# Performance work log

Hardware: AMD Instinct MI355X
Metric: run time of the kernel (lower is better)

Reference implementation:

```python
import jax, jax.numpy as jnp
import numpy as np

R = 16            # filter radius (init kwarg r)
EPS = 0.01        # regularizer (init kwarg eps)
B, H, W, C, K = 2, 1024, 1024, 3, 4


def _make_kernel():
    # Gaussian kernel with theta_alpha = r/4, center tap zeroed (as in source)
    x, y = np.mgrid[-R:R + 1, -R:R + 1]
    theta = R / 4.0
    k = np.exp(-0.5 * (x ** 2 + y ** 2) / theta ** 2).astype(np.float32)
    k[R, R] = 0.0
    return jnp.asarray(k)


def setup_inputs() -> dict:
    key = jax.random.key(0)
    k1, k2 = jax.random.split(key)
    I = jax.random.uniform(k1, (B, H, W, C), dtype=jnp.float32)
    p = jax.random.uniform(k2, (B, H, W, K), dtype=jnp.float32)
    return {"I": I, "p": p}


def _gaussian_filter(src, kfft):
    # FFT-based 'same' convolution with the (2R+1)^2 Gaussian kernel over (h, w).
    # src: [b, h, w, *trailing]; filtering applied independently per trailing channel.
    shp = src.shape
    b, h, w = shp[0], shp[1], shp[2]
    s = src.reshape(b, h, w, -1)
    s = jnp.pad(s, ((0, 0), (R, R), (R, R), (0, 0)))          # [b, h+2R, w+2R, c]
    sf = jnp.fft.rfft2(s, axes=(1, 2))
    d = jnp.fft.irfft2(sf * kfft[None, :, :, None], s=(h + 2 * R, w + 2 * R), axes=(1, 2))
    d = d[:, 2 * R:, 2 * R:, :]                               # crop back to [b, h, w, c]
    return d.reshape(shp)


def _guided_filter(I, p):
    b, h, w, c = I.shape
    k = _make_kernel()
    ext_k = jnp.pad(k, ((0, h - 1), (0, w - 1)))              # [h+2R, w+2R]
    kfft = jnp.fft.rfft2(ext_k)
    gf = lambda x: _gaussian_filter(x, kfft)

    N = gf(jnp.ones((1, h, w, 1), I.dtype))                   # normalization map
    mean_I = gf(I) / N                                        # [b,h,w,c]
    mean_p = gf(p) / N                                        # [b,h,w,k]
    # cov(I, p): [b,h,w,c,k]
    cov_Ip = gf(I[..., :, None] * p[..., None, :]) / N[..., None] \
        - mean_I[..., :, None] * mean_p[..., None, :]
    # var(I): [b,h,w,c,c]
    var_I = gf(I[..., :, None] * I[..., None, :]) / N[..., None] \
        - mean_I[..., :, None] * mean_I[..., None, :]
    A = var_I + EPS * jnp.eye(c, dtype=I.dtype)
    a = jnp.linalg.solve(A, cov_Ip)                           # == inv(A) @ cov_Ip, [b,h,w,c,k]
    b_ = mean_p[..., None] - jnp.einsum('bhwck,bhwc->bhwk', a, mean_I)[..., None]  # [b,h,w,k,1]
    mean_a = gf(a) / N[..., None]
    mean_b = gf(b_) / N[..., None]
    q = jnp.einsum('bhwck,bhwc->bhwk', mean_a, I)[..., None] + mean_b
    return q.reshape(p.shape)


def reference(I, p):
    return _guided_filter(I, p)
```

## Files before the change

kernel.cpp:

```cpp
#include <hip/hip_runtime.h>


#define HH 1024
#define WW 1024
#define HWSZ (HH * WW)
#define RR 16
#define NT 33
#define EPSF 0.01f

#define VBY 32
#define VROWS (VBY + 2 * RR)
#define VCOLS 256

typedef unsigned short u16;
typedef unsigned int u32;
typedef float v2f __attribute__((ext_vector_type(2)));

__device__ constexpr float WG[NT] = {
  0.000335463f, 0.000883827f, 0.002187492f, 0.005086072f, 0.011108997f,
  0.022794173f, 0.043936928f, 0.079559512f, 0.135335283f, 0.216265076f,
  0.324652467f, 0.457833362f, 0.606530660f, 0.754839602f, 0.882496903f,
  0.969233234f, 1.0f,         0.969233234f, 0.882496903f, 0.754839602f,
  0.606530660f, 0.457833362f, 0.324652467f, 0.216265076f, 0.135335283f,
  0.079559512f, 0.043936928f, 0.022794173f, 0.011108997f, 0.005086072f,
  0.002187492f, 0.000883827f, 0.000335463f
};

__device__ constexpr float wg_sum() {
  float s = 0.0f;
  for (int i = 0; i < NT; ++i) s += WG[i];
  return s;
}

__device__ __forceinline__ u16 f2bf(float f) {
  u32 u = __float_as_uint(f);
  u += 0x7fffu + ((u >> 16) & 1u);
  return (u16)(u >> 16);
}
__device__ __forceinline__ float bf2f(u16 v) { return __uint_as_float(((u32)v) << 16); }

__device__ __forceinline__ float win_w(int u, int n) {
  constexpr float S = wg_sum();
  if (u >= RR && u < n - RR) return S;
  float w = 0.0f;
#pragma unroll
  for (int i = 0; i < NT; ++i) {
    const int uu = u - RR + i;
    if (uu >= 0 && uu < n) w += WG[i];
  }
  return w;
}

__global__ __launch_bounds__(256) void k_prod_hblur(const float* __restrict__ I,
                                                    const float* __restrict__ P,
                                                    u16* __restrict__ HB) {
  __shared__ float sI[3][288];
  __shared__ float sp[4][288];
  const int tid = threadIdx.x;
  const int y = blockIdx.y;
  const int x0 = blockIdx.x * 256;
  {
    const int base = (y * WW + (x0 - RR)) * 3;
    for (int idx = tid; idx < 288 * 3; idx += 256) {
      const int xi = idx / 3;
      const int c = idx - xi * 3;
      const int xx = x0 - RR + xi;
      sI[c][xi] = (xx >= 0 && xx < WW) ? I[base + idx] : 0.0f;
    }
  }
  {
    const int base = (y * WW + (x0 - RR)) * 4;
    for (int idx = tid; idx < 288 * 4; idx += 256) {
      const int xi = idx >> 2;
      const int c = idx & 3;
      const int xx = x0 - RR + xi;
      sp[c][xi] = (xx >= 0 && xx < WW) ? P[base + idx] : 0.0f;
    }
  }
  __syncthreads();

  float acc[25];
#pragma unroll
  for (int j = 0; j < 25; ++j) acc[j] = 0.0f;

#pragma unroll
  for (int dx = 0; dx < NT; ++dx) {
    const float w = WG[dx];
    const float i0 = sI[0][tid + dx], i1 = sI[1][tid + dx], i2 = sI[2][tid + dx];
    const float p0 = sp[0][tid + dx], p1 = sp[1][tid + dx];
    const float p2 = sp[2][tid + dx], p3 = sp[3][tid + dx];
    const float wi0 = w * i0, wi1 = w * i1, wi2 = w * i2;
    const float wp0 = w * p0, wp1 = w * p1, wp2 = w * p2, wp3 = w * p3;
    acc[0] += wi0; acc[1] += wi1; acc[2] += wi2;
    acc[3] += wp0; acc[4] += wp1; acc[5] += wp2; acc[6] += wp3;
    acc[7]  += i0 * wp0; acc[8]  += i0 * wp1; acc[9]  += i0 * wp2; acc[10] += i0 * wp3;
    acc[11] += i1 * wp0; acc[12] += i1 * wp1; acc[13] += i1 * wp2; acc[14] += i1 * wp3;
    acc[15] += i2 * wp0; acc[16] += i2 * wp1; acc[17] += i2 * wp2; acc[18] += i2 * wp3;
    acc[19] += wi0 * i0; acc[20] += wi0 * i1; acc[21] += wi0 * i2;
    acc[22] += wi1 * i1; acc[23] += wi1 * i2; acc[24] += wi2 * i2;
  }
  const int o = y * WW + x0 + tid;
#pragma unroll
  for (int ch = 0; ch < 25; ++ch) HB[ch * HWSZ + o] = f2bf(acc[ch]);
}

__global__ __launch_bounds__(256) void k_vblur25(const u16* __restrict__ HB,
                                                 u16* __restrict__ M) {
  __shared__ u16 s[VROWS][VCOLS];
  const int tid = threadIdx.x;
  const int ch = blockIdx.z;
  const int xb = blockIdx.x * VCOLS;
  const int y0 = blockIdx.y * VBY;
  const int x = xb + tid;

  {
    const u16* src = HB + (size_t)ch * HWSZ + xb;
    uint4 tmp[8];
#pragma unroll
    for (int it = 0; it < 8; ++it) {
      const int id = it * 256 + tid;
      const int row = id >> 5;
      const int cir = id & 31;
      const int gy = y0 - RR + row;
      uint4 v = make_uint4(0u, 0u, 0u, 0u);
      if (gy >= 0 && gy < HH)
        v = *reinterpret_cast<const uint4*>(src + (size_t)gy * WW + cir * 8);
      tmp[it] = v;
    }
#pragma unroll
    for (int it = 0; it < 8; ++it) {
      const int id = it * 256 + tid;
      const int row = id >> 5;
      const int cir = id & 31;
      *reinterpret_cast<uint4*>(&s[row][cir * 8]) = tmp[it];
    }
  }
  __syncthreads();

  u16* dst = M + (size_t)ch * HWSZ;

  for (int c = 0; c < 4; ++c) {
    v2f a[4];
#pragma unroll
    for (int q = 0; q < 4; ++q) a[q] = (v2f){0.0f, 0.0f};
#pragma unroll
    for (int r = 0; r < 40; ++r) {
      const float v = bf2f(s[8 * c + r][tid]);
#pragma unroll
      for (int q = 0; q < 4; ++q) {
        const int dy0 = r - 2 * q;
        const int dy1 = r - 2 * q - 1;
        const float wa = (dy0 >= 0 && dy0 < NT) ? WG[dy0] : 0.0f;
        const float wb = (dy1 >= 0 && dy1 < NT) ? WG[dy1] : 0.0f;
        if (wa != 0.0f || wb != 0.0f) {
          const v2f w = {wa, wb};
          a[q] += w * v;
        }
      }
    }
#pragma unroll
    for (int q = 0; q < 4; ++q) {
      const int yy = y0 + 8 * c + 2 * q;
      dst[yy * WW + x] = f2bf(a[q].x);
      dst[(yy + 1) * WW + x] = f2bf(a[q].y);
    }
  }
}

__global__ __launch_bounds__(256) void k_solve(const u16* __restrict__ M,
                                               const float* __restrict__ I,
                                               const float* __restrict__ P,
                                               float* __restrict__ AB,
                                               float* __restrict__ S0) {
  const int i = blockIdx.x * 256 + threadIdx.x;
  const int y = i >> 10;
  const int x = i & 1023;
  const float invN = __builtin_amdgcn_rcpf(win_w(x, WW) * win_w(y, HH) - 1.0f);

  const float I0 = I[i * 3], I1 = I[i * 3 + 1], I2 = I[i * 3 + 2];
  float p[4];
#pragma unroll
  for (int k = 0; k < 4; ++k) p[k] = P[i * 4 + k];

  const float mI0 = (bf2f(M[i]) - I0) * invN;
  const float mI1 = (bf2f(M[HWSZ + i]) - I1) * invN;
  const float mI2 = (bf2f(M[2 * HWSZ + i]) - I2) * invN;
  float mp[4];
#pragma unroll
  for (int k = 0; k < 4; ++k) mp[k] = (bf2f(M[(3 + k) * HWSZ + i]) - p[k]) * invN;
  float cov[12];
#pragma unroll
  for (int k = 0; k < 4; ++k) {
    cov[k]     = (bf2f(M[(7 + k) * HWSZ + i])  - I0 * p[k]) * invN - mI0 * mp[k];
    cov[4 + k] = (bf2f(M[(11 + k) * HWSZ + i]) - I1 * p[k]) * invN - mI1 * mp[k];
    cov[8 + k] = (bf2f(M[(15 + k) * HWSZ + i]) - I2 * p[k]) * invN - mI2 * mp[k];
  }
  const float A00 = (bf2f(M[19 * HWSZ + i]) - I0 * I0) * invN - mI0 * mI0 + EPSF;
  const float A01 = (bf2f(M[20 * HWSZ + i]) - I0 * I1) * invN - mI0 * mI1;
  const float A02 = (bf2f(M[21 * HWSZ + i]) - I0 * I2) * invN - mI0 * mI2;
  const float A11 = (bf2f(M[22 * HWSZ + i]) - I1 * I1) * invN - mI1 * mI1 + EPSF;
  const float A12 = (bf2f(M[23 * HWSZ + i]) - I1 * I2) * invN - mI1 * mI2;
  const float A22 = (bf2f(M[24 * HWSZ + i]) - I2 * I2) * invN - mI2 * mI2 + EPSF;
  const float c00 = A11 * A22 - A12 * A12;
  const float c01 = A02 * A12 - A01 * A22;
  const float c02 = A01 * A12 - A02 * A11;
  const float det = A00 * c00 + A01 * c01 + A02 * c02;
  const float idet = 1.0f / det;
  const float i00 = c00 * idet, i01 = c01 * idet, i02 = c02 * idet;
  const float i11 = (A00 * A22 - A02 * A02) * idet;
  const float i12 = (A01 * A02 - A00 * A12) * idet;
  const float i22 = (A00 * A11 - A01 * A01) * idet;
  float4 s0;
  float* s0p = &s0.x;
#pragma unroll
  for (int k = 0; k < 4; ++k) {
    const float a0 = i00 * cov[k] + i01 * cov[4 + k] + i02 * cov[8 + k];
    const float a1 = i01 * cov[k] + i11 * cov[4 + k] + i12 * cov[8 + k];
    const float a2 = i02 * cov[k] + i12 * cov[4 + k] + i22 * cov[8 + k];
    const float b = mp[k] - (a0 * mI0 + a1 * mI1 + a2 * mI2);
    AB[k * HWSZ + i] = a0;
    AB[(4 + k) * HWSZ + i] = a1;
    AB[(8 + k) * HWSZ + i] = a2;
    AB[(12 + k) * HWSZ + i] = b;
    s0p[k] = a0 * I0 + a1 * I1 + a2 * I2 + b;
  }
  *reinterpret_cast<float4*>(S0 + (size_t)i * 4) = s0;
}

__global__ __launch_bounds__(256) void k_hblur16(const float* __restrict__ AB,
                                                 u16* __restrict__ HB) {
  __shared__ float s[1056];
  const int tid = threadIdx.x;
  const int y = blockIdx.x;
  const int ch = blockIdx.y;
  const float* src = AB + (size_t)ch * HWSZ + y * WW;
  if (tid < 16) { s[tid] = 0.0f; s[1040 + tid] = 0.0f; }
  *reinterpret_cast<float4*>(&s[16 + 4 * tid]) =
      *reinterpret_cast<const float4*>(&src[4 * tid]);
  __syncthreads();

  float vals[36];
  {
    const float4* s4 = reinterpret_cast<const float4*>(s) + tid;
#pragma unroll
    for (int r = 0; r < 9; ++r) {
      const float4 q = s4[r];
      vals[4 * r] = q.x; vals[4 * r + 1] = q.y;
      vals[4 * r + 2] = q.z; vals[4 * r + 3] = q.w;
    }
  }
  float acc[4] = {0.0f, 0.0f, 0.0f, 0.0f};
#pragma unroll
  for (int r = 0; r < 36; ++r) {
#pragma unroll
    for (int k = 0; k < 4; ++k) {
      const int dy = r - k;
      if (dy >= 0 && dy < NT) acc[k] += WG[dy] * vals[r];
    }
  }
  const u32 lo = (u32)f2bf(acc[0]) | ((u32)f2bf(acc[1]) << 16);
  const u32 hi = (u32)f2bf(acc[2]) | ((u32)f2bf(acc[3]) << 16);
  *reinterpret_cast<uint2*>(&HB[(size_t)ch * HWSZ + y * WW + 4 * tid]) =
      make_uint2(lo, hi);
}

__global__ __launch_bounds__(256) void k_vblur16(const u16* __restrict__ HB,
                                                 u16* __restrict__ MB) {
  __shared__ u16 s[VROWS][VCOLS];
  const int tid = threadIdx.x;
  const int ch = blockIdx.z;
  const int xb = blockIdx.x * VCOLS;
  const int y0 = blockIdx.y * VBY;
  const int x = xb + tid;

  {
    const u16* src = HB + (size_t)ch * HWSZ + xb;
    uint4 tmp[8];
#pragma unroll
    for (int it = 0; it < 8; ++it) {
      const int id = it * 256 + tid;
      const int row = id >> 5;
      const int cir = id & 31;
      const int gy = y0 - RR + row;
      uint4 v = make_uint4(0u, 0u, 0u, 0u);
      if (gy >= 0 && gy < HH)
        v = *reinterpret_cast<const uint4*>(src + (size_t)gy * WW + cir * 8);
      tmp[it] = v;
    }
#pragma unroll
    for (int it = 0; it < 8; ++it) {
      const int id = it * 256 + tid;
      const int row = id >> 5;
      const int cir = id & 31;
      *reinterpret_cast<uint4*>(&s[row][cir * 8]) = tmp[it];
    }
  }
  __syncthreads();

  u16* dst = MB + (size_t)ch * HWSZ;

  for (int c = 0; c < 4; ++c) {
    v2f a[4];
#pragma unroll
    for (int q = 0; q < 4; ++q) a[q] = (v2f){0.0f, 0.0f};
#pragma unroll
    for (int r = 0; r < 40; ++r) {
      const float v = bf2f(s[8 * c + r][tid]);
#pragma unroll
      for (int q = 0; q < 4; ++q) {
        const int dy0 = r - 2 * q;
        const int dy1 = r - 2 * q - 1;
        const float wa = (dy0 >= 0 && dy0 < NT) ? WG[dy0] : 0.0f;
        const float wb = (dy1 >= 0 && dy1 < NT) ? WG[dy1] : 0.0f;
        if (wa != 0.0f || wb != 0.0f) {
          const v2f w = {wa, wb};
          a[q] += w * v;
        }
      }
    }
#pragma unroll
    for (int q = 0; q < 4; ++q) {
      const int yy = y0 + 8 * c + 2 * q;
      dst[yy * WW + x] = f2bf(a[q].x);
      dst[(yy + 1) * WW + x] = f2bf(a[q].y);
    }
  }
}

__global__ __launch_bounds__(256) void k_combine(const u16* __restrict__ MB,
                                                 const float* __restrict__ S0,
                                                 const float* __restrict__ I,
                                                 float* __restrict__ out) {
  const int i = blockIdx.x * 256 + threadIdx.x;
  const int y = i >> 10;
  const int x = i & 1023;
  const float invN = __builtin_amdgcn_rcpf(win_w(x, WW) * win_w(y, HH) - 1.0f);
  float m[16];
#pragma unroll
  for (int ch = 0; ch < 16; ++ch) m[ch] = bf2f(MB[(size_t)ch * HWSZ + i]);
  const float i0 = I[i * 3], i1 = I[i * 3 + 1], i2 = I[i * 3 + 2];
  const float4 s0 = *reinterpret_cast<const float4*>(S0 + (size_t)i * 4);
  float4 q;
  q.x = (m[0] * i0 + m[4] * i1 + m[8]  * i2 + m[12] - s0.x) * invN;
  q.y = (m[1] * i0 + m[5] * i1 + m[9]  * i2 + m[13] - s0.y) * invN;
  q.z = (m[2] * i0 + m[6] * i1 + m[10] * i2 + m[14] - s0.z) * invN;
  q.w = (m[3] * i0 + m[7] * i1 + m[11] * i2 + m[15] - s0.w) * invN;
  *reinterpret_cast<float4*>(out + (size_t)i * 4) = q;
}

extern "C" void kernel_launch(void* const* d_in, const int* in_sizes, int n_in,
                              void* d_out, int out_size, void* d_ws, size_t ws_size,
                              hipStream_t stream) {
  const float* I = (const float*)d_in[0];
  const float* P = (const float*)d_in[1];
  float* out = (float*)d_out;
  float* buf0 = (float*)d_ws;
  float* buf1 = buf0 + 25 * (size_t)HWSZ;

  u16* hb1 = (u16*)buf0;
  u16* Mb  = (u16*)buf1;
  float* AB = buf0;
  float* S0 = buf0 + 16 * (size_t)HWSZ;
  u16* hb2 = (u16*)buf1;
  u16* MBp = (u16*)buf1 + 16 * (size_t)HWSZ;

  for (int b = 0; b < 2; ++b) {
    const float* Ib = I + (size_t)b * HWSZ * 3;
    const float* Pb = P + (size_t)b * HWSZ * 4;
    float* outb = out + (size_t)b * HWSZ * 4;

    k_prod_hblur<<<dim3(WW / 256, HH), dim3(256), 0, stream>>>(Ib, Pb, hb1);
    k_vblur25<<<dim3(WW / VCOLS, HH / VBY, 25), dim3(256), 0, stream>>>(hb1, Mb);
    k_solve<<<dim3(HWSZ / 256), dim3(256), 0, stream>>>(Mb, Ib, Pb, AB, S0);
    k_hblur16<<<dim3(HH, 16), dim3(256), 0, stream>>>(AB, hb2);
    k_vblur16<<<dim3(WW / VCOLS, HH / VBY, 16), dim3(256), 0, stream>>>(hb2, MBp);
    k_combine<<<dim3(HWSZ / 256), dim3(256), 0, stream>>>(MBp, S0, Ib, outb);
  }
}
```

Measured before the change: 299.3 us.

## Split product computation from horizontal blur and store intermediates in bf16

The fused product-plus-horizontal-blur kernel is replaced by a separate pointwise kernel that writes all 25 product planes in bf16, followed by a generic bf16 horizontal blur shared with the second pass. The solve kernel now writes the a/b coefficients as bf16 instead of fp32, which halves that traffic, and the two vertical-blur kernels are merged into one. The aim is to drop the heavy per-tap product arithmetic and strided input loads of the fused kernel. In exchange it adds an extra full write and read of 25 bf16 planes plus one more launch per batch, and it rounds the products and coefficients to bf16 before blurring, which costs accuracy.

```diff
diff --git a/kernel.cpp b/kernel.cpp
--- a/kernel.cpp
+++ b/kernel.cpp
@@ -51,61 +51,84 @@
   return w;
 }
 
-__global__ __launch_bounds__(256) void k_prod_hblur(const float* __restrict__ I,
-                                                    const float* __restrict__ P,
-                                                    u16* __restrict__ HB) {
-  __shared__ float sI[3][288];
-  __shared__ float sp[4][288];
+__global__ __launch_bounds__(256) void k_products(const float* __restrict__ I,
+                                                  const float* __restrict__ P,
+                                                  u16* __restrict__ PR) {
+  const int t = blockIdx.x * 256 + threadIdx.x;
+  const float2* i2 = reinterpret_cast<const float2*>(I);
+  const float2 a = i2[3 * t], b = i2[3 * t + 1], c = i2[3 * t + 2];
+  const float4* p4 = reinterpret_cast<const float4*>(P);
+  const float4 q0 = p4[2 * t], q1 = p4[2 * t + 1];
+
+  const float iA[3] = {a.x, a.y, b.x};
+  const float iB[3] = {b.y, c.x, c.y};
+  const float pA[4] = {q0.x, q0.y, q0.z, q0.w};
+  const float pB[4] = {q1.x, q1.y, q1.z, q1.w};
+
+  u32* dst = reinterpret_cast<u32*>(PR) + t;
+  const int half = HWSZ / 2;
+#define ST(ch, va, vb) dst[(ch) * half] = (u32)f2bf(va) | ((u32)f2bf(vb) << 16)
+  ST(0, iA[0], iB[0]); ST(1, iA[1], iB[1]); ST(2, iA[2], iB[2]);
+  ST(3, pA[0], pB[0]); ST(4, pA[1], pB[1]); ST(5, pA[2], pB[2]); ST(6, pA[3], pB[3]);
+#pragma unroll
+  for (int cc = 0; cc < 3; ++cc)
+#pragma unroll
+    for (int k = 0; k < 4; ++k)
+      ST(7 + cc * 4 + k, iA[cc] * pA[k], iB[cc] * pB[k]);
+  ST(19, iA[0] * iA[0], iB[0] * iB[0]);
+  ST(20, iA[0] * iA[1], iB[0] * iB[1]);
+  ST(21, iA[0] * iA[2], iB[0] * iB[2]);
+  ST(22, iA[1] * iA[1], iB[1] * iB[1]);
+  ST(23, iA[1] * iA[2], iB[1] * iB[2]);
+  ST(24, iA[2] * iA[2], iB[2] * iB[2]);
+#undef ST
+}
+
+template <int NPL>
+__global__ __launch_bounds__(256) void k_hblur_bf(const u16* __restrict__ SRC,
+                                                  u16* __restrict__ DST) {
+  __shared__ float s[1056];
   const int tid = threadIdx.x;
-  const int y = blockIdx.y;
-  const int x0 = blockIdx.x * 256;
+  const int y = blockIdx.x;
+  const int ch = blockIdx.y;
+  const u16* src = SRC + (size_t)ch * HWSZ + y * WW;
+  if (tid < 16) { s[tid] = 0.0f; s[1040 + tid] = 0.0f; }
   {
-    const int base = (y * WW + (x0 - RR)) * 3;
-    for (int idx = tid; idx < 288 * 3; idx += 256) {
-      const int xi = idx / 3;
-      const int c = idx - xi * 3;
-      const int xx = x0 - RR + xi;
-      sI[c][xi] = (xx >= 0 && xx < WW) ? I[base + idx] : 0.0f;
-    }
-  }
+    const uint2 v = *reinterpret_cast<const uint2*>(src + 4 * tid);
+    s[16 + 4 * tid]     = bf2f((u16)v.x);
+    s[16 + 4 * tid + 1] = bf2f((u16)(v.x >> 16));
+    s[16 + 4 * tid + 2] = bf2f((u16)v.y);
+    s[16 + 4 * tid + 3] = bf2f((u16)(v.y >> 16));
+  }
+  __syncthreads();
+
+  float vals[36];
   {
-    const int base = (y * WW + (x0 - RR)) * 4;
-    for (int idx = tid; idx < 288 * 4; idx += 256) {
-      const int xi = idx >> 2;
-      const int c = idx & 3;
-      const int xx = x0 - RR + xi;
-      sp[c][xi] = (xx >= 0 && xx < WW) ? P[base + idx] : 0.0f;
-    }
-  }
-  __syncthreads();
-
-  float acc[25];
-#pragma unroll
-  for (int j = 0; j < 25; ++j) acc[j] = 0.0f;
-
-#pragma unroll
-  for (int dx = 0; dx < NT; ++dx) {
-    const float w = WG[dx];
-    const float i0 = sI[0][tid + dx], i1 = sI[1][tid + dx], i2 = sI[2][tid + dx];
-    const float p0 = sp[0][tid + dx], p1 = sp[1][tid + dx];
-    const float p2 = sp[2][tid + dx], p3 = sp[3][tid + dx];
-    const float wi0 = w * i0, wi1 = w * i1, wi2 = w * i2;
-    const float wp0 = w * p0, wp1 = w * p1, wp2 = w * p2, wp3 = w * p3;
-    acc[0] += wi0; acc[1] += wi1; acc[2] += wi2;
-    acc[3] += wp0; acc[4] += wp1; acc[5] += wp2; acc[6] += wp3;
-    acc[7]  += i0 * wp0; acc[8]  += i0 * wp1; acc[9]  += i0 * wp2; acc[10] += i0 * wp3;
-    acc[11] += i1 * wp0; acc[12] += i1 * wp1; acc[13] += i1 * wp2; acc[14] += i1 * wp3;
-    acc[15] += i2 * wp0; acc[16] += i2 * wp1; acc[17] += i2 * wp2; acc[18] += i2 * wp3;
-    acc[19] += wi0 * i0; acc[20] += wi0 * i1; acc[21] += wi0 * i2;
-    acc[22] += wi1 * i1; acc[23] += wi1 * i2; acc[24] += wi2 * i2;
-  }
-  const int o = y * WW + x0 + tid;
-#pragma unroll
-  for (int ch = 0; ch < 25; ++ch) HB[ch * HWSZ + o] = f2bf(acc[ch]);
-}
-
-__global__ __launch_bounds__(256) void k_vblur25(const u16* __restrict__ HB,
-                                                 u16* __restrict__ M) {
+    const float4* s4 = reinterpret_cast<const float4*>(s) + tid;
+#pragma unroll
+    for (int r = 0; r < 9; ++r) {
+      const float4 q = s4[r];
+      vals[4 * r] = q.x; vals[4 * r + 1] = q.y;
+      vals[4 * r + 2] = q.z; vals[4 * r + 3] = q.w;
+    }
+  }
+  float acc[4] = {0.0f, 0.0f, 0.0f, 0.0f};
+#pragma unroll
+  for (int r = 0; r < 36; ++r) {
+#pragma unroll
+    for (int k = 0; k < 4; ++k) {
+      const int dy = r - k;
+      if (dy >= 0 && dy < NT) acc[k] += WG[dy] * vals[r];
+    }
+  }
+  const u32 lo = (u32)f2bf(acc[0]) | ((u32)f2bf(acc[1]) << 16);
+  const u32 hi = (u32)f2bf(acc[2]) | ((u32)f2bf(acc[3]) << 16);
+  *reinterpret_cast<uint2*>(&DST[(size_t)ch * HWSZ + y * WW + 4 * tid]) =
+      make_uint2(lo, hi);
+}
+
+__global__ __launch_bounds__(256) void k_vblur(const u16* __restrict__ HB,
+                                               u16* __restrict__ M) {
   __shared__ u16 s[VROWS][VCOLS];
   const int tid = threadIdx.x;
   const int ch = blockIdx.z;
@@ -170,7 +193,7 @@
 __global__ __launch_bounds__(256) void k_solve(const u16* __restrict__ M,
                                                const float* __restrict__ I,
                                                const float* __restrict__ P,
-                                               float* __restrict__ AB,
+                                               u16* __restrict__ AB,
                                                float* __restrict__ S0) {
   const int i = blockIdx.x * 256 + threadIdx.x;
   const int y = i >> 10;
@@ -218,113 +241,13 @@
     const float a1 = i01 * cov[k] + i11 * cov[4 + k] + i12 * cov[8 + k];
     const float a2 = i02 * cov[k] + i12 * cov[4 + k] + i22 * cov[8 + k];
     const float b = mp[k] - (a0 * mI0 + a1 * mI1 + a2 * mI2);
-    AB[k * HWSZ + i] = a0;
-    AB[(4 + k) * HWSZ + i] = a1;
-    AB[(8 + k) * HWSZ + i] = a2;
-    AB[(12 + k) * HWSZ + i] = b;
+    AB[k * HWSZ + i] = f2bf(a0);
+    AB[(4 + k) * HWSZ + i] = f2bf(a1);
+    AB[(8 + k) * HWSZ + i] = f2bf(a2);
+    AB[(12 + k) * HWSZ + i] = f2bf(b);
     s0p[k] = a0 * I0 + a1 * I1 + a2 * I2 + b;
   }
   *reinterpret_cast<float4*>(S0 + (size_t)i * 4) = s0;
-}
-
-__global__ __launch_bounds__(256) void k_hblur16(const float* __restrict__ AB,
-                                                 u16* __restrict__ HB) {
-  __shared__ float s[1056];
-  const int tid = threadIdx.x;
-  const int y = blockIdx.x;
-  const int ch = blockIdx.y;
-  const float* src = AB + (size_t)ch * HWSZ + y * WW;
-  if (tid < 16) { s[tid] = 0.0f; s[1040 + tid] = 0.0f; }
-  *reinterpret_cast<float4*>(&s[16 + 4 * tid]) =
-      *reinterpret_cast<const float4*>(&src[4 * tid]);
-  __syncthreads();
-
-  float vals[36];
-  {
-    const float4* s4 = reinterpret_cast<const float4*>(s) + tid;
-#pragma unroll
-    for (int r = 0; r < 9; ++r) {
-      const float4 q = s4[r];
-      vals[4 * r] = q.x; vals[4 * r + 1] = q.y;
-      vals[4 * r + 2] = q.z; vals[4 * r + 3] = q.w;
-    }
-  }
-  float acc[4] = {0.0f, 0.0f, 0.0f, 0.0f};
-#pragma unroll
-  for (int r = 0; r < 36; ++r) {
-#pragma unroll
-    for (int k = 0; k < 4; ++k) {
-      const int dy = r - k;
-      if (dy >= 0 && dy < NT) acc[k] += WG[dy] * vals[r];
-    }
-  }
-  const u32 lo = (u32)f2bf(acc[0]) | ((u32)f2bf(acc[1]) << 16);
-  const u32 hi = (u32)f2bf(acc[2]) | ((u32)f2bf(acc[3]) << 16);
-  *reinterpret_cast<uint2*>(&HB[(size_t)ch * HWSZ + y * WW + 4 * tid]) =
-      make_uint2(lo, hi);
-}
-
-__global__ __launch_bounds__(256) void k_vblur16(const u16* __restrict__ HB,
-                                                 u16* __restrict__ MB) {
-  __shared__ u16 s[VROWS][VCOLS];
-  const int tid = threadIdx.x;
-  const int ch = blockIdx.z;
-  const int xb = blockIdx.x * VCOLS;
-  const int y0 = blockIdx.y * VBY;
-  const int x = xb + tid;
-
-  {
-    const u16* src = HB + (size_t)ch * HWSZ + xb;
-    uint4 tmp[8];
-#pragma unroll
-    for (int it = 0; it < 8; ++it) {
-      const int id = it * 256 + tid;
-      const int row = id >> 5;
-      const int cir = id & 31;
-      const int gy = y0 - RR + row;
-      uint4 v = make_uint4(0u, 0u, 0u, 0u);
-      if (gy >= 0 && gy < HH)
-        v = *reinterpret_cast<const uint4*>(src + (size_t)gy * WW + cir * 8);
-      tmp[it] = v;
-    }
-#pragma unroll
-    for (int it = 0; it < 8; ++it) {
-      const int id = it * 256 + tid;
-      const int row = id >> 5;
-      const int cir = id & 31;
-      *reinterpret_cast<uint4*>(&s[row][cir * 8]) = tmp[it];
-    }
-  }
-  __syncthreads();
-
-  u16* dst = MB + (size_t)ch * HWSZ;
-
-  for (int c = 0; c < 4; ++c) {
-    v2f a[4];
-#pragma unroll
-    for (int q = 0; q < 4; ++q) a[q] = (v2f){0.0f, 0.0f};
-#pragma unroll
-    for (int r = 0; r < 40; ++r) {
-      const float v = bf2f(s[8 * c + r][tid]);
-#pragma unroll
-      for (int q = 0; q < 4; ++q) {
-        const int dy0 = r - 2 * q;
-        const int dy1 = r - 2 * q - 1;
-        const float wa = (dy0 >= 0 && dy0 < NT) ? WG[dy0] : 0.0f;
-        const float wb = (dy1 >= 0 && dy1 < NT) ? WG[dy1] : 0.0f;
-        if (wa != 0.0f || wb != 0.0f) {
-          const v2f w = {wa, wb};
-          a[q] += w * v;
-        }
-      }
-    }
-#pragma unroll
-    for (int q = 0; q < 4; ++q) {
-      const int yy = y0 + 8 * c + 2 * q;
-      dst[yy * WW + x] = f2bf(a[q].x);
-      dst[(yy + 1) * WW + x] = f2bf(a[q].y);
-    }
-  }
 }
 
 __global__ __launch_bounds__(256) void k_combine(const u16* __restrict__ MB,
@@ -357,23 +280,25 @@
   float* buf0 = (float*)d_ws;
   float* buf1 = buf0 + 25 * (size_t)HWSZ;
 
-  u16* hb1 = (u16*)buf0;
-  u16* Mb  = (u16*)buf1;
-  float* AB = buf0;
-  float* S0 = buf0 + 16 * (size_t)HWSZ;
-  u16* hb2 = (u16*)buf1;
-  u16* MBp = (u16*)buf1 + 16 * (size_t)HWSZ;
+  u16* PR  = (u16*)buf0;
+  u16* Mb  = (u16*)buf0;
+  u16* HB2 = (u16*)buf0;
+  u16* MBp = (u16*)buf0 + 16 * (size_t)HWSZ;
+  u16* HB1 = (u16*)buf1;
+  u16* AB  = (u16*)buf1;
+  float* S0 = buf1 + 8 * (size_t)HWSZ;
 
   for (int b = 0; b < 2; ++b) {
     const float* Ib = I + (size_t)b * HWSZ * 3;
     const float* Pb = P + (size_t)b * HWSZ * 4;
     float* outb = out + (size_t)b * HWSZ * 4;
 
-    k_prod_hblur<<<dim3(WW / 256, HH), dim3(256), 0, stream>>>(Ib, Pb, hb1);
-    k_vblur25<<<dim3(WW / VCOLS, HH / VBY, 25), dim3(256), 0, stream>>>(hb1, Mb);
+    k_products<<<dim3(HWSZ / 512), dim3(256), 0, stream>>>(Ib, Pb, PR);
+    k_hblur_bf<25><<<dim3(HH, 25), dim3(256), 0, stream>>>(PR, HB1);
+    k_vblur<<<dim3(WW / VCOLS, HH / VBY, 25), dim3(256), 0, stream>>>(HB1, Mb);
     k_solve<<<dim3(HWSZ / 256), dim3(256), 0, stream>>>(Mb, Ib, Pb, AB, S0);
-    k_hblur16<<<dim3(HH, 16), dim3(256), 0, stream>>>(AB, hb2);
-    k_vblur16<<<dim3(WW / VCOLS, HH / VBY, 16), dim3(256), 0, stream>>>(hb2, MBp);
+    k_hblur_bf<16><<<dim3(HH, 16), dim3(256), 0, stream>>>(AB, HB2);
+    k_vblur<<<dim3(WW / VCOLS, HH / VBY, 16), dim3(256), 0, stream>>>(HB2, MBp);
     k_combine<<<dim3(HWSZ / 256), dim3(256), 0, stream>>>(MBp, S0, Ib, outb);
   }
 }
```

After: 302.7 us. No clear change (+1.1%).
